# Performance work log

Measured on AMD Instinct MI355X. Metric: run time of the kernel, lower is better.

Reference implementation:

```python
import jax, jax.numpy as jnp
import numpy as np
import math

N_HEAD = 16
HEAD_QKV = 1024  # total qkv width; head_dim = HEAD_QKV // N_HEAD
WM_DECAY_LENGTH = 2048
WM_DECAY_RATE = 1.0
WM_ECHOIC = 16


def decay_weight_matrix(n):
    # power_law decay, faithful to get_decay_weight_matrix
    dl = WM_DECAY_LENGTH - WM_ECHOIC + 1
    nums = jnp.linspace(0.0, 1.0, dl)
    decay_values = 1.0 - jnp.power(nums, 1.0 / (np.e * WM_DECAY_RATE))
    decay_values = jnp.concatenate([jnp.ones(WM_ECHOIC - 1), decay_values])  # [WM_DECAY_LENGTH]
    decay_values = decay_values[:n]
    idx = jnp.arange(n)[:, None] - jnp.arange(n)[None, :]  # [n,n], negative above diag
    mat = decay_values[jnp.clip(idx, 0, n - 1)]
    return jnp.tril(mat).astype(jnp.float32)


def setup_inputs() -> dict:
    key = jax.random.key(0)
    k1, k2, k3 = jax.random.split(key, 3)
    B, T, C = 2, 2048, 1024
    x = jax.random.normal(k1, (B, T, C), dtype=jnp.float32)
    W_attn = jax.random.normal(k2, (C, 3 * HEAD_QKV), dtype=jnp.float32) * (1.0 / math.sqrt(C))
    W_proj = jax.random.normal(k3, (HEAD_QKV, C), dtype=jnp.float32) * (1.0 / math.sqrt(HEAD_QKV))
    return {"x": x, "W_attn": W_attn, "W_proj": W_proj}


def reference(x, W_attn, W_proj):
    B, T, C = x.shape
    hd = HEAD_QKV // N_HEAD
    qkv = x @ W_attn  # [B,T,3*HEAD_QKV]
    q, k, v = jnp.split(qkv, 3, axis=-1)
    # [B,T,HQKV] -> [B,H,T,hd]
    q = q.reshape(B, T, N_HEAD, hd).transpose(0, 2, 1, 3)
    k = k.reshape(B, T, N_HEAD, hd).transpose(0, 2, 1, 3)
    v = v.reshape(B, T, N_HEAD, hd).transpose(0, 2, 1, 3)
    att = jnp.einsum('bhqd,bhkd->bhqk', q, k) * (1.0 / math.sqrt(hd))
    causal = jnp.tril(jnp.ones((T, T), dtype=bool))
    att = jnp.where(causal, att, -jnp.inf)
    att = jax.nn.softmax(att, axis=-1)
    att = att * decay_weight_matrix(T)  # post-softmax multiplicative decay
    y = jnp.einsum('bhqk,bhkd->bhqd', att, v)
    y = y.transpose(0, 2, 1, 3).reshape(B, T, HEAD_QKV)
    return y @ W_proj
```

## Files before the change

kernel.cpp:

```cpp
#include <hip/hip_runtime.h>
#include <math.h>

#define B_  2
#define T_  2048
#define C_  1024
#define NH_ 16
#define HD_ 64
#define N3_ 3072

typedef float f32x4 __attribute__((ext_vector_type(4)));
typedef short bf16x8 __attribute__((ext_vector_type(8)));
typedef unsigned short u16;
typedef float f32x4_base __attribute__((ext_vector_type(4)));
typedef f32x4_base __attribute__((aligned(4))) f32x4u;

#define QSCALE 0.18033688011112042f

#if __has_builtin(__builtin_amdgcn_exp2f)
#define EXP2(x) __builtin_amdgcn_exp2f(x)
#else
#define EXP2(x) exp2f(x)
#endif

__device__ __forceinline__ u16 f2bf(float x) {
  unsigned int u = __builtin_bit_cast(unsigned int, x);
  u += 0x7FFFu + ((u >> 16) & 1u);
  return (u16)(u >> 16);
}

__device__ __forceinline__ unsigned int cvt_pk_bf16(float lo, float hi) {
  unsigned int r;
  asm("v_cvt_pk_bf16_f32 %0, %1, %2" : "=v"(r) : "v"(lo), "v"(hi));
  return r;
}

#define GLD16(g, l) __builtin_amdgcn_global_load_lds( \
    (__attribute__((address_space(1))) void*)(g), \
    (__attribute__((address_space(3))) void*)(l), 16, 0, 0)

__global__ __launch_bounds__(256) void prep_kernel(
    const float* __restrict__ x, u16* __restrict__ xb,
    const float* __restrict__ Wa, u16* __restrict__ WaT,
    const float* __restrict__ Wp, u16* __restrict__ WpT,
    float* __restrict__ decR)
{
  __shared__ float tile[32][33];
  const int bid = blockIdx.x;
  const int tid = threadIdx.x;
  if (bid < 4096) {
    int i = (bid * 256 + tid) * 4;
    float4 v = *(const float4*)(x + i);
    ushort4 o;
    o.x = f2bf(v.x); o.y = f2bf(v.y); o.z = f2bf(v.z); o.w = f2bf(v.w);
    *(ushort4*)(xb + i) = o;
  } else if (bid < 8192) {
    const float* in; u16* out; int Cc, c0, r0;
    if (bid < 7168) {
      int t = bid - 4096;
      in = Wa; out = WaT; Cc = N3_;
      c0 = (t % 96) * 32; r0 = (t / 96) * 32;
    } else {
      int t = bid - 7168;
      in = Wp; out = WpT; Cc = C_;
      c0 = (t % 32) * 32; r0 = (t / 32) * 32;
    }
    int tx = tid & 31, ty = tid >> 5;
#pragma unroll
    for (int rr = ty; rr < 32; rr += 8)
      tile[rr][tx] = in[(size_t)(r0 + rr) * Cc + c0 + tx];
    __syncthreads();
#pragma unroll
    for (int rr = ty; rr < 32; rr += 8)
      out[(size_t)(c0 + rr) * 1024 + r0 + tx] = f2bf(tile[tx][rr]);
  } else {
    int j = (bid - 8192) * 256 + tid;
    if (j < 4352) {
      int d = 2047 - j;
      float v = 1.0f;
      if (d >= 15) v = 1.0f - powf((float)(d - 15) * (1.0f / 2032.0f), 0.36787944117144233f);
      decR[j] = v;
    }
  }
}

template<int MODE>
__global__ __launch_bounds__(256, 3) void gemm128_kernel(
    const u16* __restrict__ A, const u16* __restrict__ Bt,
    float* __restrict__ Cf, u16* __restrict__ Cq, u16* __restrict__ Vt,
    int M, int N, int K)
{
  __shared__ char lds[49152];
  const int lane = threadIdx.x & 63;
  const int wave = threadIdx.x >> 6;
  const int nxb = N >> 7;
  const int orig = blockIdx.x;
  const int cpx = (int)gridDim.x >> 3;
  const int wg = (orig & 7) * cpx + (orig >> 3);
  const int m0 = (wg / nxb) << 7;
  const int n0 = (wg % nxb) << 7;
  const int wm = wave >> 1, wn = wave & 1;

  f32x4 acc[4][4] = {};

#define GSTAGE(buf, k0)                                                          \
  {                                                                              \
    _Pragma("unroll")                                                            \
    for (int c = 0; c < 2; ++c) {                                                \
      int chunk = wave * 2048 + c * 1024;                                        \
      int row = (chunk >> 6) + (lane >> 2);                                      \
      int wb = ((lane & 3) << 4) ^ ((row & 3) << 4);                             \
      GLD16((const char*)(A  + (size_t)(m0 + row) * K + (k0)) + wb,              \
            lds + (buf) * 16384 + chunk);                                        \
      GLD16((const char*)(Bt + (size_t)(n0 + row) * K + (k0)) + wb,              \
            lds + (buf) * 16384 + 8192 + chunk);                                 \
    }                                                                            \
  }

  const int nk = K >> 5;
  GSTAGE(0, 0);
  GSTAGE(1, 32);
  __syncthreads();

  for (int i = 0; i < nk; ++i) {
    if (i + 1 < nk) asm volatile("s_waitcnt vmcnt(4)" ::: "memory");
    else            asm volatile("s_waitcnt vmcnt(0)" ::: "memory");
    __builtin_amdgcn_s_barrier();
    __builtin_amdgcn_sched_barrier(0);
    if (i + 2 < nk) GSTAGE((i + 2) % 3, (i + 2) * 32);

    const char* base = lds + (i % 3) * 16384;
    bf16x8 af[4], bfr[4];
#pragma unroll
    for (int m = 0; m < 4; ++m) {
      int row = wm * 64 + m * 16 + (lane & 15);
      int wb = ((lane >> 4) << 4) ^ ((row & 3) << 4);
      af[m] = *(const bf16x8*)(base + row * 64 + wb);
    }
#pragma unroll
    for (int n = 0; n < 4; ++n) {
      int row = wn * 64 + n * 16 + (lane & 15);
      int wb = ((lane >> 4) << 4) ^ ((row & 3) << 4);
      bfr[n] = *(const bf16x8*)(base + 8192 + row * 64 + wb);
    }
    __builtin_amdgcn_s_setprio(1);
#pragma unroll
    for (int m = 0; m < 4; ++m)
#pragma unroll
      for (int n = 0; n < 4; ++n)
        acc[m][n] = __builtin_amdgcn_mfma_f32_16x16x32_bf16(af[m], bfr[n], acc[m][n], 0, 0, 0);
    __builtin_amdgcn_s_setprio(0);
  }

#pragma unroll
  for (int m = 0; m < 4; ++m) {
    int grow0 = m0 + wm * 64 + m * 16 + ((lane >> 4) << 2);
#pragma unroll
    for (int n = 0; n < 4; ++n) {
      int gcol = n0 + wn * 64 + n * 16 + (lane & 15);
      f32x4 v = acc[m][n];
      if (MODE == 0) {
        int bb = grow0 >> 11, tt0 = grow0 & 2047;
        int which = gcol >> 10, rem = gcol & 1023;
        int hh = rem >> 6, dd = rem & 63;
        if (which < 2) {
#pragma unroll
          for (int r = 0; r < 4; ++r) {
            float ov = (which == 0) ? v[r] * QSCALE : v[r];
            Cq[((size_t)(which * 32 + bb * 16 + hh) * 2048 + tt0 + r) * 64 + dd] = f2bf(ov);
          }
        } else {
          ushort4 o;
          o.x = f2bf(v[0]); o.y = f2bf(v[1]); o.z = f2bf(v[2]); o.w = f2bf(v[3]);
          *(ushort4*)(Vt + ((size_t)(bb * 16 + hh) * 64 + dd) * 2048 + tt0) = o;
        }
      } else {
#pragma unroll
        for (int r = 0; r < 4; ++r)
          Cf[(size_t)(grow0 + r) * N + gcol] = v[r];
      }
    }
  }
#undef GSTAGE
}

__global__ __launch_bounds__(256, 2) void attn_kernel(
    const u16* __restrict__ qkb, const u16* __restrict__ vtg,
    const float* __restrict__ decR, u16* __restrict__ yb)
{
  __shared__ char klds[2][8192];
  __shared__ char vlds[2][8192];
  __shared__ u16 plds[64 * 76];

  const int lane = threadIdx.x & 63;
  const int wave = threadIdx.x >> 6;
  const int quad = lane >> 4;
  const int l15 = lane & 15;
  const int orig = blockIdx.x;
  const int xcd = orig & 7;
  const int bh = xcd * 4 + ((orig >> 3) & 3);
  const int x = orig >> 5;
  const int qtA = x;
  const int qtB = 31 - x;
  const int b = bh >> 4, h = bh & 15;

  const u16* Q   = qkb + (size_t)bh * T_ * HD_;
  const u16* Kg  = qkb + (size_t)(32 + bh) * T_ * HD_;
  const u16* VTg = vtg + (size_t)bh * HD_ * T_;

  const int wrowB = qtB * 64 + wave * 16;
  const int wrowA = qtA * 64 + wave * 16;
  const int qB = wrowB + l15;
  const int qA = wrowA + l15;
  const float* dpB = decR + (2047 - qB + quad * 4);
  const float* dpA = decR + (2047 - qA + quad * 4);

  bf16x8 qaB[2], qaA[2];
  { const u16* qp = Q + (size_t)qB * HD_ + quad * 8;
    qaB[0] = *(const bf16x8*)qp; qaB[1] = *(const bf16x8*)(qp + 32); }
  { const u16* qp = Q + (size_t)qA * HD_ + quad * 8;
    qaA[0] = *(const bf16x8*)qp; qaA[1] = *(const bf16x8*)(qp + 32); }

  f32x4 accB[4] = {}, accA[4] = {};
  float lsumB = 0.0f, lsumA = 0.0f;

#define ASTAGE(buf, kt)                                                          \
  {                                                                              \
    _Pragma("unroll")                                                            \
    for (int c = 0; c < 2; ++c) {                                                \
      int chunk = wave * 2048 + c * 1024;                                        \
      int row = (chunk >> 7) + (lane >> 3);                                      \
      int wb = ((lane & 7) << 4) ^ ((row & 7) << 4);                             \
      GLD16((const char*)(Kg + (size_t)((kt) * 64 + row) * HD_) + wb,            \
            klds[buf] + chunk);                                                  \
      GLD16((const char*)(VTg + (size_t)row * T_ + (kt) * 64) + wb,              \
            vlds[buf] + chunk);                                                  \
    }                                                                            \
  }

  const int twoA1 = 2 * qtA + 1;

  f32x4 dc[4], dn[4];
#pragma unroll
  for (int f = 0; f < 4; ++f) dn[f] = *(const f32x4u*)(dpB + f * 16);
  ASTAGE(0, 0);
  __syncthreads();

  for (int u = 0; u < 33; ++u) {
    const int kt   = (u <= twoA1) ? (u >> 1) : (u - qtA - 1);
    const int selA = (u <= twoA1) ? (u & 1) : 0;
    const int cur  = kt & 1;

#pragma unroll
    for (int f = 0; f < 4; ++f) dc[f] = dn[f];
    {
      const int u1 = u + 1;
      const int kt1   = (u1 <= twoA1) ? (u1 >> 1) : (u1 - qtA - 1);
      const int selA1 = (u1 <= twoA1) ? (u1 & 1) : 0;
      const float* dnp = (selA1 ? dpA : dpB) + kt1 * 64;
#pragma unroll
      for (int f = 0; f < 4; ++f) dn[f] = *(const f32x4u*)(dnp + f * 16);
    }

    asm volatile("s_waitcnt vmcnt(8)" ::: "memory");
    __builtin_amdgcn_s_barrier();
    __builtin_amdgcn_sched_barrier(0);
    if (!selA && kt < qtB) ASTAGE(cur ^ 1, kt + 1);

    bf16x8 kf[4][2];
#pragma unroll
    for (int f = 0; f < 4; ++f) {
      int krow = f * 16 + l15;
      int base = krow * 128;
      int msk = (krow & 7) << 4;
      kf[f][0] = *(const bf16x8*)(klds[cur] + base + ((quad * 16) ^ msk));
      kf[f][1] = *(const bf16x8*)(klds[cur] + base + ((64 + quad * 16) ^ msk));
    }

    const bf16x8 q0 = selA ? qaA[0] : qaB[0];
    const bf16x8 q1 = selA ? qaA[1] : qaB[1];
    f32x4 s[4];
    __builtin_amdgcn_s_setprio(1);
#pragma unroll
    for (int f = 0; f < 4; ++f) {
      f32x4 t = {};
      t = __builtin_amdgcn_mfma_f32_16x16x32_bf16(kf[f][0], q0, t, 0, 0, 0);
      t = __builtin_amdgcn_mfma_f32_16x16x32_bf16(kf[f][1], q1, t, 0, 0, 0);
      s[f] = t;
    }
    __builtin_amdgcn_s_setprio(0);

    const int qtsel = selA ? qtA : qtB;
    if (kt == qtsel) {
      const int qsel = selA ? qA : qB;
#pragma unroll
      for (int f = 0; f < 4; ++f) {
        int key0 = kt * 64 + f * 16 + quad * 4;
#pragma unroll
        for (int r = 0; r < 4; ++r)
          if (key0 + r > qsel) s[f][r] = -1e30f;
      }
    }

    float ls = 0.0f;
#pragma unroll
    for (int f = 0; f < 4; ++f) {
      f32x4 p;
#pragma unroll
      for (int r = 0; r < 4; ++r) p[r] = EXP2(s[f][r]);
      ls += (p[0] + p[1]) + (p[2] + p[3]);
      unsigned int w0 = cvt_pk_bf16(p[0] * dc[f][0], p[1] * dc[f][1]);
      unsigned int w1 = cvt_pk_bf16(p[2] * dc[f][2], p[3] * dc[f][3]);
      uint2 wv; wv.x = w0; wv.y = w1;
      *(uint2*)(plds + (size_t)(wave * 16 + l15) * 76 + f * 16 + quad * 4) = wv;
    }
    if (selA) lsumA += ls; else lsumB += ls;

    bf16x8 vf[4][2];
#pragma unroll
    for (int n = 0; n < 4; ++n) {
      int vrow = n * 16 + l15;
      int mskv = (vrow & 7) << 4;
#pragma unroll
      for (int ks = 0; ks < 2; ++ks)
        vf[n][ks] = *(const bf16x8*)(vlds[cur] + vrow * 128 + ((ks * 64 + quad * 16) ^ mskv));
    }

    bf16x8 pa0 = *(const bf16x8*)(plds + (size_t)(wave * 16 + l15) * 76 + quad * 8);
    bf16x8 pa1 = *(const bf16x8*)(plds + (size_t)(wave * 16 + l15) * 76 + 32 + quad * 8);
    __builtin_amdgcn_s_setprio(1);
    if (selA) {
#pragma unroll
      for (int n = 0; n < 4; ++n) {
        accA[n] = __builtin_amdgcn_mfma_f32_16x16x32_bf16(pa0, vf[n][0], accA[n], 0, 0, 0);
        accA[n] = __builtin_amdgcn_mfma_f32_16x16x32_bf16(pa1, vf[n][1], accA[n], 0, 0, 0);
      }
    } else {
#pragma unroll
      for (int n = 0; n < 4; ++n) {
        accB[n] = __builtin_amdgcn_mfma_f32_16x16x32_bf16(pa0, vf[n][0], accB[n], 0, 0, 0);
        accB[n] = __builtin_amdgcn_mfma_f32_16x16x32_bf16(pa1, vf[n][1], accB[n], 0, 0, 0);
      }
    }
    __builtin_amdgcn_s_setprio(0);
  }
#undef ASTAGE

  lsumB += __shfl_xor(lsumB, 16); lsumB += __shfl_xor(lsumB, 32);
  lsumA += __shfl_xor(lsumA, 16); lsumA += __shfl_xor(lsumA, 32);
  float rB[4], rA[4];
#pragma unroll
  for (int r = 0; r < 4; ++r) {
    rB[r] = 1.0f / __shfl(lsumB, quad * 4 + r, 16);
    rA[r] = 1.0f / __shfl(lsumA, quad * 4 + r, 16);
  }
#pragma unroll
  for (int n = 0; n < 4; ++n) {
    int d = h * 64 + n * 16 + l15;
#pragma unroll
    for (int r = 0; r < 4; ++r) {
      int tB = wrowB + quad * 4 + r;
      int tA = wrowA + quad * 4 + r;
      yb[((size_t)b * T_ + tB) * 1024 + d] = f2bf(accB[n][r] * rB[r]);
      yb[((size_t)b * T_ + tA) * 1024 + d] = f2bf(accA[n][r] * rA[r]);
    }
  }
}

extern "C" void kernel_launch(void* const* d_in, const int* in_sizes, int n_in,
                              void* d_out, int out_size, void* d_ws, size_t ws_size,
                              hipStream_t stream) {
  const float* x  = (const float*)d_in[0];
  const float* Wa = (const float*)d_in[1];
  const float* Wp = (const float*)d_in[2];
  float* out = (float*)d_out;
  char* ws = (char*)d_ws;

  u16*   xb    = (u16*)(ws + 0);
  u16*   WaT   = (u16*)(ws + 8388608);
  u16*   WpT   = (u16*)(ws + 14680064);
  u16*   qkb   = (u16*)(ws + 16777216);
  float* decR  = (float*)(ws + 33554432);
  u16*   VT    = (u16*)(ws + 41943040);
  u16*   yb    = xb;

  prep_kernel<<<8209, 256, 0, stream>>>(x, xb, Wa, WaT, Wp, WpT, decR);
  gemm128_kernel<0><<<768, 256, 0, stream>>>(
      xb, WaT, nullptr, qkb, VT, B_ * T_, N3_, C_);
  attn_kernel<<<512, 256, 0, stream>>>(qkb, VT, decR, yb);
  gemm128_kernel<1><<<256, 256, 0, stream>>>(
      yb, WpT, out, nullptr, nullptr, B_ * T_, 1024, 1024);
}
```

Baseline: 103.8 us.

## Replace QKV GEMM with 256x256-tile, 8-wave kernel using phased LDS pipeline

The QKV projection GEMM now uses a new 256x256 tile kernel with 512 threads and 128KB of dynamic LDS. It double-buffers A and B tiles and interleaves global loads across four compute phases per k-tile. The larger tiles raise data reuse per block and cut global traffic, at the cost of one block per CU and only 192 blocks on the grid. The attention kernel's vmcnt wait threshold is also lowered from 8 to 4.

```diff
diff --git a/kernel.cpp b/kernel.cpp
--- a/kernel.cpp
+++ b/kernel.cpp
@@ -83,11 +83,137 @@
   }
 }
 
-template<int MODE>
+__global__ void __launch_bounds__(512, 1) gemm256_kernel(
+    const u16* __restrict__ A, const u16* __restrict__ Bt,
+    u16* __restrict__ Cq, u16* __restrict__ Vt,
+    int M, int N, int K)
+{
+  extern __shared__ char lds[];
+  const int tid = threadIdx.x;
+  const int lane = tid & 63;
+  const int wave = tid >> 6;
+  const int wm = wave >> 2;
+  const int wn = wave & 3;
+  const int quad = lane >> 4;
+  const int l15 = lane & 15;
+  const int nxb = N >> 8;
+  const int orig = blockIdx.x;
+  const int cpx = (int)gridDim.x >> 3;
+  const int wg = (orig & 7) * cpx + (orig >> 3);
+  const int m0 = (wg / nxb) << 8;
+  const int n0 = (wg % nxb) << 8;
+
+  f32x4 acc[8][4] = {};
+
+  const int abase = wm * 16384;
+  const int bbase = 65536 + (wn >> 1) * 16384;
+  const int brow0 = (wn & 1) * 64;
+
+#define HSTAGE(arr, rowbase, tile, ldsoff)                                       \
+  {                                                                              \
+    _Pragma("unroll")                                                            \
+    for (int p = 0; p < 2; ++p) {                                                \
+      int chunk = p * 8192 + tid * 16;                                           \
+      int row = chunk >> 7;                                                      \
+      int colb = (chunk & 127) ^ ((row & 7) << 4);                               \
+      GLD16((const char*)((arr) + (size_t)((rowbase) + row) * K + (size_t)(tile) * 64) + colb, \
+            lds + (ldsoff) + chunk);                                             \
+    }                                                                            \
+  }
+
+#define PHASE(mg, buf, BLOAD, WAIT, STAGE_STMT)                                  \
+  {                                                                              \
+    if (WAIT) asm volatile("s_waitcnt vmcnt(4)" ::: "memory");                   \
+    __builtin_amdgcn_s_barrier();                                                \
+    __builtin_amdgcn_sched_barrier(0);                                           \
+    STAGE_STMT;                                                                  \
+    if (BLOAD) {                                                                 \
+      _Pragma("unroll")                                                          \
+      for (int n = 0; n < 4; ++n) {                                              \
+        int rl = brow0 + n * 16 + l15;                                           \
+        int msk = (rl & 7) << 4;                                                 \
+        bfr[n][0] = *(const bf16x8*)(lds + bbase + (buf) * 32768 + rl * 128 +    \
+                                     ((quad * 16) ^ msk));                       \
+        bfr[n][1] = *(const bf16x8*)(lds + bbase + (buf) * 32768 + rl * 128 +    \
+                                     ((64 + quad * 16) ^ msk));                  \
+      }                                                                          \
+    }                                                                            \
+    bf16x8 af[2][2];                                                             \
+    _Pragma("unroll")                                                            \
+    for (int mm = 0; mm < 2; ++mm) {                                             \
+      int rl = (mg) * 32 + mm * 16 + l15;                                        \
+      int msk = (rl & 7) << 4;                                                   \
+      af[mm][0] = *(const bf16x8*)(lds + abase + (buf) * 32768 + rl * 128 +      \
+                                   ((quad * 16) ^ msk));                         \
+      af[mm][1] = *(const bf16x8*)(lds + abase + (buf) * 32768 + rl * 128 +      \
+                                   ((64 + quad * 16) ^ msk));                    \
+    }                                                                            \
+    __builtin_amdgcn_s_setprio(1);                                               \
+    _Pragma("unroll")                                                            \
+    for (int mm = 0; mm < 2; ++mm)                                               \
+      _Pragma("unroll")                                                          \
+      for (int n = 0; n < 4; ++n) {                                              \
+        acc[(mg) * 2 + mm][n] = __builtin_amdgcn_mfma_f32_16x16x32_bf16(         \
+            af[mm][0], bfr[n][0], acc[(mg) * 2 + mm][n], 0, 0, 0);               \
+        acc[(mg) * 2 + mm][n] = __builtin_amdgcn_mfma_f32_16x16x32_bf16(         \
+            af[mm][1], bfr[n][1], acc[(mg) * 2 + mm][n], 0, 0, 0);               \
+      }                                                                          \
+    __builtin_amdgcn_s_setprio(0);                                               \
+  }
+
+  bf16x8 bfr[4][2];
+
+  HSTAGE(Bt, n0 + 0,   0, 65536 + 0);
+  HSTAGE(Bt, n0 + 128, 0, 65536 + 16384);
+  HSTAGE(A,  m0 + 0,   0, 0);
+  HSTAGE(A,  m0 + 128, 0, 16384);
+  HSTAGE(Bt, n0 + 0,   1, 65536 + 32768);
+  HSTAGE(Bt, n0 + 128, 1, 65536 + 32768 + 16384);
+
+  const int nt = K >> 6;
+  const int tm = nt - 1;
+  for (int j = 0; j < nt / 2; ++j) {
+    const int t1 = 2 * j + 1, t2 = (2 * j + 2) & tm, t3 = (2 * j + 3) & tm;
+    PHASE(0, 0, true,  true,  HSTAGE(A, m0 + 0,   t1, 32768));
+    PHASE(1, 0, false, false, HSTAGE(A, m0 + 128, t1, 32768 + 16384));
+    PHASE(2, 0, false, false, HSTAGE(Bt, n0 + 0,   t2, 65536));
+    PHASE(3, 0, false, false, HSTAGE(Bt, n0 + 128, t2, 65536 + 16384));
+    PHASE(0, 1, true,  true,  HSTAGE(A, m0 + 0,   t2, 0));
+    PHASE(1, 1, false, false, HSTAGE(A, m0 + 128, t2, 16384));
+    PHASE(2, 1, false, false, HSTAGE(Bt, n0 + 0,   t3, 65536 + 32768));
+    PHASE(3, 1, false, false, HSTAGE(Bt, n0 + 128, t3, 65536 + 32768 + 16384));
+  }
+#undef PHASE
+#undef HSTAGE
+
+#pragma unroll
+  for (int m = 0; m < 8; ++m) {
+    int grow0 = m0 + wm * 128 + m * 16 + quad * 4;
+#pragma unroll
+    for (int n = 0; n < 4; ++n) {
+      int gcol = n0 + wn * 64 + n * 16 + l15;
+      f32x4 v = acc[m][n];
+      int bb = grow0 >> 11, tt0 = grow0 & 2047;
+      int which = gcol >> 10, rem = gcol & 1023;
+      int hh = rem >> 6, dd = rem & 63;
+      if (which < 2) {
+#pragma unroll
+        for (int r = 0; r < 4; ++r) {
+          float ov = (which == 0) ? v[r] * QSCALE : v[r];
+          Cq[((size_t)(which * 32 + bb * 16 + hh) * 2048 + tt0 + r) * 64 + dd] = f2bf(ov);
+        }
+      } else {
+        ushort4 o;
+        o.x = f2bf(v[0]); o.y = f2bf(v[1]); o.z = f2bf(v[2]); o.w = f2bf(v[3]);
+        *(ushort4*)(Vt + ((size_t)(bb * 16 + hh) * 64 + dd) * 2048 + tt0) = o;
+      }
+    }
+  }
+}
+
 __global__ __launch_bounds__(256, 3) void gemm128_kernel(
     const u16* __restrict__ A, const u16* __restrict__ Bt,
-    float* __restrict__ Cf, u16* __restrict__ Cq, u16* __restrict__ Vt,
-    int M, int N, int K)
+    float* __restrict__ Cf, int M, int N, int K)
 {
   __shared__ char lds[49152];
   const int lane = threadIdx.x & 63;
@@ -158,26 +284,9 @@
     for (int n = 0; n < 4; ++n) {
       int gcol = n0 + wn * 64 + n * 16 + (lane & 15);
       f32x4 v = acc[m][n];
-      if (MODE == 0) {
-        int bb = grow0 >> 11, tt0 = grow0 & 2047;
-        int which = gcol >> 10, rem = gcol & 1023;
-        int hh = rem >> 6, dd = rem & 63;
-        if (which < 2) {
-#pragma unroll
-          for (int r = 0; r < 4; ++r) {
-            float ov = (which == 0) ? v[r] * QSCALE : v[r];
-            Cq[((size_t)(which * 32 + bb * 16 + hh) * 2048 + tt0 + r) * 64 + dd] = f2bf(ov);
-          }
-        } else {
-          ushort4 o;
-          o.x = f2bf(v[0]); o.y = f2bf(v[1]); o.z = f2bf(v[2]); o.w = f2bf(v[3]);
-          *(ushort4*)(Vt + ((size_t)(bb * 16 + hh) * 64 + dd) * 2048 + tt0) = o;
-        }
-      } else {
-#pragma unroll
-        for (int r = 0; r < 4; ++r)
-          Cf[(size_t)(grow0 + r) * N + gcol] = v[r];
-      }
+#pragma unroll
+      for (int r = 0; r < 4; ++r)
+        Cf[(size_t)(grow0 + r) * N + gcol] = v[r];
     }
   }
 #undef GSTAGE
@@ -261,7 +370,7 @@
       for (int f = 0; f < 4; ++f) dn[f] = *(const f32x4u*)(dnp + f * 16);
     }
 
-    asm volatile("s_waitcnt vmcnt(8)" ::: "memory");
+    asm volatile("s_waitcnt vmcnt(4)" ::: "memory");
     __builtin_amdgcn_s_barrier();
     __builtin_amdgcn_sched_barrier(0);
     if (!selA && kt < qtB) ASTAGE(cur ^ 1, kt + 1);
@@ -383,10 +492,11 @@
   u16*   VT    = (u16*)(ws + 41943040);
   u16*   yb    = xb;
 
+  hipFuncSetAttribute((const void*)gemm256_kernel,
+                      hipFuncAttributeMaxDynamicSharedMemorySize, 131072);
+
   prep_kernel<<<8209, 256, 0, stream>>>(x, xb, Wa, WaT, Wp, WpT, decR);
-  gemm128_kernel<0><<<768, 256, 0, stream>>>(
-      xb, WaT, nullptr, qkb, VT, B_ * T_, N3_, C_);
+  gemm256_kernel<<<192, 512, 131072, stream>>>(xb, WaT, qkb, VT, B_ * T_, N3_, C_);
   attn_kernel<<<512, 256, 0, stream>>>(qkb, VT, decR, yb);
-  gemm128_kernel<1><<<256, 256, 0, stream>>>(
-      yb, WpT, out, nullptr, nullptr, B_ * T_, 1024, 1024);
-}
+  gemm128_kernel<<<256, 256, 0, stream>>>(yb, WpT, out, B_ * T_, 1024, 1024);
+}
```

After: 101.2 us. -2.6%, faster.
